# Performance work log

Measured on AMD Instinct MI355X. Metric: run time of the kernel, lower is better.

The kernel has to match this reference:

```python
import jax, jax.numpy as jnp
import numpy as np

B, S, DM, H, DF = 2, 2048, 1024, 16, 4096
HD = DM // H
EPS = 1e-6
NEG = -1e9


def setup_inputs() -> dict:
    key = jax.random.key(0)
    ks = jax.random.split(key, 16)
    sc = 1.0 / np.sqrt(DM)
    scf = 1.0 / np.sqrt(DF)
    return {
        "x": jax.random.normal(ks[0], (B, S, DM), jnp.float32),
        "src_mask": jax.random.randint(ks[1], (B, 1, 1, S), 0, 2, jnp.int32),
        "Wq": jax.random.normal(ks[2], (DM, DM), jnp.float32) * sc,
        "bq": jnp.zeros((DM,), jnp.float32),
        "Wk": jax.random.normal(ks[3], (DM, DM), jnp.float32) * sc,
        "bk": jnp.zeros((DM,), jnp.float32),
        "Wv": jax.random.normal(ks[4], (DM, DM), jnp.float32) * sc,
        "bv": jnp.zeros((DM,), jnp.float32),
        "Wo": jax.random.normal(ks[5], (DM, DM), jnp.float32) * sc,
        "bo": jnp.zeros((DM,), jnp.float32),
        "W1": jax.random.normal(ks[6], (DM, DF), jnp.float32) * sc,
        "b1": jnp.zeros((DF,), jnp.float32),
        "W2": jax.random.normal(ks[7], (DF, DM), jnp.float32) * scf,
        "b2": jnp.zeros((DM,), jnp.float32),
        "alpha1": jnp.ones((1,), jnp.float32),
        "beta1": jnp.ones((1,), jnp.float32),
        "alpha2": jnp.ones((1,), jnp.float32),
        "beta2": jnp.ones((1,), jnp.float32),
    }


def layer_norm(x, alpha, beta):
    # torch: mean + unbiased std (ddof=1), scalar alpha/beta, eps added to std
    mean = jnp.mean(x, axis=-1, keepdims=True)
    std = jnp.std(x, axis=-1, keepdims=True, ddof=1)
    return alpha * (x - mean) / (std + EPS) + beta


def mha(x, mask, Wq, bq, Wk, bk, Wv, bv, Wo, bo):
    def split(t):  # [B,S,DM] -> [B,H,S,HD]
        return t.reshape(B, S, H, HD).transpose(0, 2, 1, 3)
    q = split(x @ Wq + bq)
    k = split(x @ Wk + bk)
    v = split(x @ Wv + bv)
    scores = jnp.einsum("bhqd,bhkd->bhqk", q, k) / np.sqrt(HD)
    scores = jnp.where(mask == 0, NEG, scores)
    probs = jax.nn.softmax(scores, axis=-1)  # dropout in eval mode = identity
    out = jnp.einsum("bhqk,bhkd->bhqd", probs, v)
    out = out.transpose(0, 2, 1, 3).reshape(B, S, DM)
    return out @ Wo + bo


def reference(x, src_mask, Wq, bq, Wk, bk, Wv, bv, Wo, bo, W1, b1, W2, b2,
              alpha1, beta1, alpha2, beta2):
    # pre-norm residual: x + attn(norm(x)); dropout disabled (eval)
    n1 = layer_norm(x, alpha1, beta1)
    h = x + mha(n1, src_mask, Wq, bq, Wk, bk, Wv, bv, Wo, bo)
    n2 = layer_norm(h, alpha2, beta2)
    ff = jax.nn.relu(n2 @ W1 + b1) @ W2 + b2
    return h + ff
```

## Files before the change

### kernel.cpp

```cpp
#include <hip/hip_runtime.h>
#include <hip/hip_bf16.h>

#define SEQ   2048
#define BATCH 2
#define DMODEL 1024
#define DFF   4096
#define NHEAD 16
#define HDIM  64
#define NTOK  (BATCH*SEQ)

typedef short s8v __attribute__((ext_vector_type(8)));
typedef float f4v __attribute__((ext_vector_type(4)));

__device__ __forceinline__ float b2f(unsigned short u) {
    union { unsigned int i; float f; } v; v.i = ((unsigned int)u) << 16; return v.f;
}
__device__ __forceinline__ unsigned short f2b(float f) {
    union { unsigned int i; float f; } v; v.f = f;
    unsigned int r = v.i + 0x7FFFu + ((v.i >> 16) & 1u);
    return (unsigned short)(r >> 16);
}
__device__ __forceinline__ ushort2 cvt_pk(float a, float b) {
    __hip_bfloat162 h = __float22bfloat162_rn(float2{ a, b });
    return *(ushort2*)&h;
}

__device__ __forceinline__ f4v mfma_bf16(s8v a, s8v b, f4v c) {
    return __builtin_amdgcn_mfma_f32_16x16x32_bf16(a, b, c, 0, 0, 0);
}

__device__ __forceinline__ void gload_lds16(const void* g, void* l) {
    __builtin_amdgcn_global_load_lds(
        (const __attribute__((address_space(1))) unsigned int*)g,
        (__attribute__((address_space(3))) unsigned int*)l, 16, 0, 0);
}

template<int N> __device__ __forceinline__ void wait_vmcnt() {
    if constexpr (N == 8)      asm volatile("s_waitcnt vmcnt(8)" ::: "memory");
    else if constexpr (N == 6) asm volatile("s_waitcnt vmcnt(6)" ::: "memory");
    else if constexpr (N == 4) asm volatile("s_waitcnt vmcnt(4)" ::: "memory");
    else if constexpr (N == 2) asm volatile("s_waitcnt vmcnt(2)" ::: "memory");
    else                       asm volatile("s_waitcnt vmcnt(0)" ::: "memory");
}

__device__ __forceinline__ void tp_tile(const float* __restrict__ src,
                                        unsigned short* __restrict__ dst,
                                        int R, int C, int br, int bc, int t,
                                        unsigned short* tl) {
    for (int i = 0; i < 4; i++) {
        int lin = i * 1024 + t * 4;
        int r = lin >> 6, c = lin & 63;
        float4 u = *(const float4*)&src[(size_t)(br * 64 + r) * C + bc * 64 + c];
        tl[r * 65 + c + 0] = f2b(u.x);
        tl[r * 65 + c + 1] = f2b(u.y);
        tl[r * 65 + c + 2] = f2b(u.z);
        tl[r * 65 + c + 3] = f2b(u.w);
    }
    __syncthreads();
    for (int i = 0; i < 4; i++) {
        int lin = i * 1024 + t * 4;
        int r2 = lin >> 6, c2 = lin & 63;
        ushort4 o;
        o.x = tl[(c2 + 0) * 65 + r2];
        o.y = tl[(c2 + 1) * 65 + r2];
        o.z = tl[(c2 + 2) * 65 + r2];
        o.w = tl[(c2 + 3) * 65 + r2];
        *(ushort4*)&dst[(size_t)(bc * 64 + r2) * R + br * 64 + c2] = o;
    }
}

__global__ __launch_bounds__(256) void prep_weights(const float* __restrict__ Wq,
                                                    const float* __restrict__ Wk,
                                                    const float* __restrict__ Wv,
                                                    const float* __restrict__ Wo,
                                                    const float* __restrict__ W1,
                                                    const float* __restrict__ W2,
                                                    const float* __restrict__ bq,
                                                    const float* __restrict__ bk,
                                                    const float* __restrict__ bv,
                                                    const float* __restrict__ x,
                                                    const float* __restrict__ a1,
                                                    const float* __restrict__ be1,
                                                    unsigned short* __restrict__ Wqkv_t,
                                                    unsigned short* __restrict__ Wo_t,
                                                    unsigned short* __restrict__ W1_t,
                                                    unsigned short* __restrict__ W2_t,
                                                    float* __restrict__ bqkv,
                                                    unsigned short* __restrict__ n1) {
    __shared__ unsigned short tl[64 * 65];
    __shared__ float red[8];
    const int t = threadIdx.x;
    const int bx = blockIdx.x, by = blockIdx.y, z = blockIdx.z;
    if (z < 4) {
        const float* src = (z == 0) ? Wq : (z == 1) ? Wk : (z == 2) ? Wv : Wo;
        unsigned short* dst = (z == 3) ? Wo_t : Wqkv_t + (size_t)z * 1024 * 1024;
        tp_tile(src, dst, 1024, 1024, bx, by, t, tl);
    } else if (z == 4) {
        for (int i = 0; i < 4; i++) {
            tp_tile(W1, W1_t, 1024, 4096, bx, by + 16 * i, t, tl);
            __syncthreads();
        }
    } else if (z == 5) {
        if (bx == 0 && by == 0) {
            for (int i = 0; i < 12; i++) {
                int idx = t + 256 * i;
                if (idx < 1024) bqkv[idx] = bq[idx];
                else if (idx < 2048) bqkv[idx] = bk[idx - 1024];
                else if (idx < 3072) bqkv[idx] = bv[idx - 2048];
            }
        }
        for (int i = 0; i < 4; i++) {
            tp_tile(W2, W2_t, 4096, 1024, bx + 16 * i, by, t, tl);
            __syncthreads();
        }
    } else {
        const int row = (z - 6) * 256 + by * 16 + bx;
        const float* xr = x + (size_t)row * DMODEL;
        float4 u = ((const float4*)xr)[t];
        float v[4] = { u.x, u.y, u.z, u.w };
        float s = v[0] + v[1] + v[2] + v[3];
        float sq = v[0]*v[0] + v[1]*v[1] + v[2]*v[2] + v[3]*v[3];
        for (int off = 32; off; off >>= 1) { s += __shfl_xor(s, off); sq += __shfl_xor(sq, off); }
        int wave = t >> 6, lane = t & 63;
        if (!lane) { red[wave] = s; red[4 + wave] = sq; }
        __syncthreads();
        s = red[0] + red[1] + red[2] + red[3];
        sq = red[4] + red[5] + red[6] + red[7];
        float mean = s * (1.f / DMODEL);
        float var = (sq - (float)DMODEL * mean * mean) * (1.f / (DMODEL - 1));
        var = var < 0.f ? 0.f : var;
        float inv = a1[0] / (sqrtf(var) + 1e-6f);
        float bt = be1[0];
        uint2 ou;
        unsigned short r0 = f2b((v[0] - mean) * inv + bt);
        unsigned short r1 = f2b((v[1] - mean) * inv + bt);
        unsigned short r2 = f2b((v[2] - mean) * inv + bt);
        unsigned short r3 = f2b((v[3] - mean) * inv + bt);
        ou.x = (unsigned int)r0 | ((unsigned int)r1 << 16);
        ou.y = (unsigned int)r2 | ((unsigned int)r3 << 16);
        ((uint2*)(n1 + (size_t)row * DMODEL))[t] = ou;
    }
}

__global__ __launch_bounds__(256) void mask_scan(const int* __restrict__ msk,
                                                 int* __restrict__ idx,
                                                 float* __restrict__ maskc2,
                                                 int* __restrict__ ntiles) {
    const int b = blockIdx.x, t = threadIdx.x;
    const int base = b * SEQ;
    __shared__ int wsum[4];
    int k[8]; int cnt = 0;
    for (int j = 0; j < 8; j++) {
        k[j] = (msk[base + t * 8 + j] != 0) ? 1 : 0;
        cnt += k[j];
    }
    const int lane = t & 63, wv = t >> 6;
    int pre = cnt;
    for (int off = 1; off < 64; off <<= 1) {
        int n = __shfl_up(pre, off);
        if (lane >= off) pre += n;
    }
    if (lane == 63) wsum[wv] = pre;
    __syncthreads();
    const int Nb = wsum[0] + wsum[1] + wsum[2] + wsum[3];
    int woff = 0;
    for (int w = 0; w < wv; w++) woff += wsum[w];
    const int excl = woff + pre - cnt;
    for (int j = 0; j < 8; j++) {
        int g = t * 8 + j;
        idx[base + g] = 0;
        maskc2[base + g] = (g < Nb) ? 0.f : -1e9f;
    }
    __syncthreads();
    int pos = excl;
    for (int j = 0; j < 8; j++) {
        if (k[j]) { idx[base + pos] = t * 8 + j; pos++; }
    }
    if (t == 0) ntiles[b] = (Nb + 63) >> 6;
}

__global__ __launch_bounds__(256) void pack_kv(const unsigned short* __restrict__ Kb,
                                               const unsigned short* __restrict__ Vb,
                                               const int* __restrict__ idx,
                                               const int* __restrict__ ntiles,
                                               unsigned short* __restrict__ Kc,
                                               unsigned short* __restrict__ Vc) {
    __shared__ unsigned short tl[64 * 65];
    const int t = threadIdx.x;
    const int kt = blockIdx.x, h = blockIdx.y, b = blockIdx.z;
    if (kt >= ntiles[b]) return;
    const int* idxb = idx + b * SEQ + kt * 64;
    const unsigned short* srcK = Kb + (size_t)b * SEQ * 1024 + h * HDIM;
    unsigned short* dstK = Kc + ((size_t)((b * NHEAD + h) * 32 + kt)) * 4096;
    for (int i = 0; i < 2; i++) {
        int ci = t + 256 * i;
        int r = ci >> 3, cp = ci & 7;
        int cl = cp ^ (r & 7);
        int row = idxb[r];
        *(uint4*)&dstK[ci * 8] = *(const uint4*)&srcK[(size_t)row * 1024 + cl * 8];
    }
    const unsigned short* srcV = Vb + (size_t)b * SEQ * 1024 + h * HDIM;
    for (int i = 0; i < 16; i++) {
        int idx2 = t + 256 * i;
        int r = idx2 >> 6, c = idx2 & 63;
        int row = idxb[r];
        tl[r * 65 + c] = srcV[(size_t)row * 1024 + c];
    }
    __syncthreads();
    unsigned short* dstV = Vc + ((size_t)((b * NHEAD + h) * 32 + kt)) * 4096;
    for (int i = 0; i < 2; i++) {
        int ci = t + 256 * i;
        int r = ci >> 3, cp = ci & 7;
        int cl = cp ^ (r & 7);
        ushort4 e0, e1;
        e0.x = tl[(cl * 8 + 0) * 65 + r]; e0.y = tl[(cl * 8 + 1) * 65 + r];
        e0.z = tl[(cl * 8 + 2) * 65 + r]; e0.w = tl[(cl * 8 + 3) * 65 + r];
        e1.x = tl[(cl * 8 + 4) * 65 + r]; e1.y = tl[(cl * 8 + 5) * 65 + r];
        e1.z = tl[(cl * 8 + 6) * 65 + r]; e1.w = tl[(cl * 8 + 7) * 65 + r];
        *(ushort4*)&dstV[ci * 8]     = e0;
        *(ushort4*)&dstV[ci * 8 + 4] = e1;
    }
}

__global__ __launch_bounds__(256) void ln_add(const float* __restrict__ x,
                                              const float* __restrict__ ws,
                                              const float* __restrict__ al,
                                              const float* __restrict__ be,
                                              float* __restrict__ hb,
                                              unsigned short* __restrict__ o) {
    const int row = blockIdx.x;
    float4 u = ((const float4*)(x + (size_t)row * DMODEL))[threadIdx.x];
    float4 p = ((const float4*)(ws + (size_t)row * DMODEL))[threadIdx.x];
    u.x += p.x; u.y += p.y; u.z += p.z; u.w += p.w;
    ((float4*)(hb + (size_t)row * DMODEL))[threadIdx.x] = u;
    float v[4] = { u.x, u.y, u.z, u.w };
    float s = v[0] + v[1] + v[2] + v[3];
    float sq = v[0]*v[0] + v[1]*v[1] + v[2]*v[2] + v[3]*v[3];
    for (int off = 32; off; off >>= 1) { s += __shfl_xor(s, off); sq += __shfl_xor(sq, off); }
    __shared__ float red[8];
    int wave = threadIdx.x >> 6, lane = threadIdx.x & 63;
    if (!lane) { red[wave] = s; red[4 + wave] = sq; }
    __syncthreads();
    s = red[0] + red[1] + red[2] + red[3];
    sq = red[4] + red[5] + red[6] + red[7];
    float mean = s * (1.f / DMODEL);
    float var = (sq - (float)DMODEL * mean * mean) * (1.f / (DMODEL - 1));
    var = var < 0.f ? 0.f : var;
    float inv = al[0] / (sqrtf(var) + 1e-6f);
    float bt = be[0];
    uint2 ou;
    unsigned short r0 = f2b((v[0] - mean) * inv + bt);
    unsigned short r1 = f2b((v[1] - mean) * inv + bt);
    unsigned short r2 = f2b((v[2] - mean) * inv + bt);
    unsigned short r3 = f2b((v[3] - mean) * inv + bt);
    ou.x = (unsigned int)r0 | ((unsigned int)r1 << 16);
    ou.y = (unsigned int)r2 | ((unsigned int)r3 << 16);
    ((uint2*)(o + (size_t)row * DMODEL))[threadIdx.x] = ou;
}


template<int SPAN, int NL>
__device__ __forceinline__ void stage_half(const unsigned short* __restrict__ mat,
                                           int base, int K, int k0, int q,
                                           unsigned short* sdst, int t) {
#pragma unroll
    for (int i = 0; i < NL; i++) {
        int ci = i * 512 + t;
        int rl = ci >> 3;
        int c  = (ci & 7) ^ (rl & 7);
        int gr = (rl / SPAN) * (2 * SPAN) + q * SPAN + (rl % SPAN);
        gload_lds16(mat + (size_t)(base + gr) * K + k0 + c * 8, sdst + (size_t)ci * 8);
    }
}

__device__ __forceinline__ const s8v* afrag(const unsigned short* sA, int mi, int s,
                                            int wm, int l16, int quad) {
    int q = mi >> 2;
    int rl = wm * 64 + (mi & 3) * 16 + l16;
    return (const s8v*)&sA[q * 8192 + rl * 64 + (((s * 4 + quad) ^ (l16 & 7)) * 8)];
}
__device__ __forceinline__ const s8v* bfrag(const unsigned short* sB, int ni, int s,
                                            int wn, int l16, int quad) {
    int q = ni >> 1;
    int rl = wn * 32 + (ni & 1) * 16 + l16;
    return (const s8v*)&sB[q * 8192 + rl * 64 + (((s * 4 + quad) ^ (l16 & 7)) * 8)];
}

__device__ __forceinline__ void half_8ph(const unsigned short* __restrict__ A,
                                         const unsigned short* __restrict__ Bt,
                                         int m0, int n0, int K, int kT1, int kT2, bool doT2,
                                         const unsigned short* sAr, const unsigned short* sBr,
                                         unsigned short* sA_this, unsigned short* sB_this,
                                         unsigned short* sA_oth,
                                         int wm, int wn, int l16, int quad, int t,
                                         f4v acc[8][4]) {
    s8v a[4][2], b[4][2];
#pragma unroll
    for (int m2 = 0; m2 < 4; m2++) {
        a[m2][0] = *afrag(sAr, m2, 0, wm, l16, quad);
        a[m2][1] = *afrag(sAr, m2, 1, wm, l16, quad);
    }
#pragma unroll
    for (int nb = 0; nb < 2; nb++) {
        b[nb][0] = *bfrag(sBr, nb, 0, wn, l16, quad);
        b[nb][1] = *bfrag(sBr, nb, 1, wn, l16, quad);
    }
    stage_half<64, 2>(A, m0, K, kT1, 1, sA_oth + 8192, t);
    __builtin_amdgcn_s_barrier();
    asm volatile("s_waitcnt lgkmcnt(0)" ::: "memory");
    __builtin_amdgcn_s_setprio(1);
#pragma unroll
    for (int m2 = 0; m2 < 4; m2++)
#pragma unroll
        for (int nb = 0; nb < 2; nb++) {
            acc[m2][nb] = mfma_bf16(a[m2][0], b[nb][0], acc[m2][nb]);
            acc[m2][nb] = mfma_bf16(a[m2][1], b[nb][1], acc[m2][nb]);
        }
    __builtin_amdgcn_s_setprio(0);
    __builtin_amdgcn_s_barrier();
#pragma unroll
    for (int nb = 0; nb < 2; nb++) {
        b[2 + nb][0] = *bfrag(sBr, 2 + nb, 0, wn, l16, quad);
        b[2 + nb][1] = *bfrag(sBr, 2 + nb, 1, wn, l16, quad);
    }
    if (doT2) stage_half<64, 2>(A, m0, K, kT2, 0, sA_this, t);
    __builtin_amdgcn_s_barrier();
    asm volatile("s_waitcnt lgkmcnt(0)" ::: "memory");
    __builtin_amdgcn_s_setprio(1);
#pragma unroll
    for (int m2 = 0; m2 < 4; m2++)
#pragma unroll
        for (int nb = 0; nb < 2; nb++) {
            acc[m2][2 + nb] = mfma_bf16(a[m2][0], b[2 + nb][0], acc[m2][2 + nb]);
            acc[m2][2 + nb] = mfma_bf16(a[m2][1], b[2 + nb][1], acc[m2][2 + nb]);
        }
    __builtin_amdgcn_s_setprio(0);
    __builtin_amdgcn_s_barrier();
#pragma unroll
    for (int m2 = 0; m2 < 4; m2++) {
        a[m2][0] = *afrag(sAr, 4 + m2, 0, wm, l16, quad);
        a[m2][1] = *afrag(sAr, 4 + m2, 1, wm, l16, quad);
    }
    if (doT2) stage_half<32, 2>(Bt, n0, K, kT2, 0, sB_this, t);
    __builtin_amdgcn_s_barrier();
    asm volatile("s_waitcnt lgkmcnt(0)" ::: "memory");
    __builtin_amdgcn_s_setprio(1);
#pragma unroll
    for (int m2 = 0; m2 < 4; m2++)
#pragma unroll
        for (int nb = 0; nb < 2; nb++) {
            acc[4 + m2][nb] = mfma_bf16(a[m2][0], b[nb][0], acc[4 + m2][nb]);
            acc[4 + m2][nb] = mfma_bf16(a[m2][1], b[nb][1], acc[4 + m2][nb]);
        }
    __builtin_amdgcn_s_setprio(0);
    __builtin_amdgcn_s_barrier();
    if (doT2) {
        stage_half<32, 2>(Bt, n0, K, kT2, 1, sB_this + 8192, t);
        wait_vmcnt<6>();
    } else {
        wait_vmcnt<0>();
    }
    __builtin_amdgcn_s_barrier();
    __builtin_amdgcn_s_setprio(1);
#pragma unroll
    for (int m2 = 0; m2 < 4; m2++)
#pragma unroll
        for (int nb = 0; nb < 2; nb++) {
            acc[4 + m2][2 + nb] = mfma_bf16(a[m2][0], b[2 + nb][0], acc[4 + m2][2 + nb]);
            acc[4 + m2][2 + nb] = mfma_bf16(a[m2][1], b[2 + nb][1], acc[4 + m2][2 + nb]);
        }
    __builtin_amdgcn_s_setprio(0);
    __builtin_amdgcn_s_barrier();
}

__device__ __forceinline__ void comp_full(const unsigned short* sA, const unsigned short* sB,
                                          int wm, int wn, int l16, int quad,
                                          f4v acc[8][4]) {
    s8v b[4][2];
#pragma unroll
    for (int ni = 0; ni < 4; ni++) {
        b[ni][0] = *bfrag(sB, ni, 0, wn, l16, quad);
        b[ni][1] = *bfrag(sB, ni, 1, wn, l16, quad);
    }
#pragma unroll
    for (int mi = 0; mi < 8; mi++) {
        s8v a0 = *afrag(sA, mi, 0, wm, l16, quad);
        s8v a1 = *afrag(sA, mi, 1, wm, l16, quad);
#pragma unroll
        for (int ni = 0; ni < 4; ni++) {
            acc[mi][ni] = mfma_bf16(a0, b[ni][0], acc[mi][ni]);
            acc[mi][ni] = mfma_bf16(a1, b[ni][1], acc[mi][ni]);
        }
    }
}

template<bool RELU, typename CT, bool SPLIT3, bool ATOM>
__global__ __launch_bounds__(512, 2) void gemm256(const unsigned short* __restrict__ A,
                                                  const unsigned short* __restrict__ Bt,
                                                  const float* __restrict__ bias,
                                                  CT* __restrict__ C,
                                                  int M, int N, int K, int KS) {
    __shared__ __align__(16) unsigned short smA[2][256 * 64];
    __shared__ __align__(16) unsigned short smB[2][256 * 64];
    const int t = threadIdx.x;
    const int wave = t >> 6, lane = t & 63;
    const int quad = lane >> 4, l16 = lane & 15;
    const int wm = wave >> 2, wn = wave & 3;
    const int m0 = blockIdx.x * 256, n0 = blockIdx.y * 256;
    const int z = blockIdx.z;
    const int kbeg = z * KS;
    const int nt = KS >> 6;

    f4v acc[8][4] = {};

    stage_half<64, 2>(A, m0, K, kbeg, 0, smA[0], t);
    stage_half<64, 2>(A, m0, K, kbeg, 1, smA[0] + 8192, t);
    stage_half<32, 2>(Bt, n0, K, kbeg, 0, smB[0], t);
    stage_half<32, 2>(Bt, n0, K, kbeg, 1, smB[0] + 8192, t);
    stage_half<64, 2>(A, m0, K, kbeg + 64, 0, smA[1], t);
    stage_half<32, 2>(Bt, n0, K, kbeg + 64, 0, smB[1], t);
    stage_half<32, 2>(Bt, n0, K, kbeg + 64, 1, smB[1] + 8192, t);
    wait_vmcnt<6>();
    __builtin_amdgcn_s_barrier();

    for (int i = 0; i < nt / 2 - 1; ++i) {
        const int kb = kbeg + 2 * i * 64;
        half_8ph(A, Bt, m0, n0, K, kb + 64, kb + 128, true,
                 smA[0], smB[0], smA[0], smB[0], smA[1],
                 wm, wn, l16, quad, t, acc);
        half_8ph(A, Bt, m0, n0, K, kb + 128, kb + 192, true,
                 smA[1], smB[1], smA[1], smB[1], smA[0],
                 wm, wn, l16, quad, t, acc);
    }
    half_8ph(A, Bt, m0, n0, K, kbeg + (nt - 1) * 64, 0, false,
             smA[0], smB[0], smA[0], smB[0], smA[1],
             wm, wn, l16, quad, t, acc);
    __builtin_amdgcn_s_setprio(1);
    comp_full(smA[1], smB[1], wm, wn, l16, quad, acc);
    __builtin_amdgcn_s_setprio(0);

#pragma unroll
    for (int mi = 0; mi < 8; mi++) {
#pragma unroll
        for (int ni = 0; ni < 4; ni++) {
            const int col = n0 + wn * 64 + ni * 16 + l16;
            const int row0 = m0 + wm * 128 + mi * 16 + quad * 4;
            const float bv = (!ATOM || z == 0) ? bias[col] : 0.f;
#pragma unroll
            for (int r = 0; r < 4; r++) {
                float v = acc[mi][ni][r] + bv;
                if (RELU) v = v > 0.f ? v : 0.f;
                if constexpr (ATOM) {
                    atomicAdd((float*)&C[(size_t)(row0 + r) * N + col], v);
                } else {
                    size_t cidx;
                    if constexpr (SPLIT3)
                        cidx = (size_t)(col >> 10) * ((size_t)NTOK * 1024)
                             + (size_t)(row0 + r) * 1024 + (col & 1023);
                    else
                        cidx = (size_t)(row0 + r) * N + col;
                    if constexpr (sizeof(CT) == 2)
                        C[cidx] = f2b(v);
                    else
                        C[cidx] = v;
                }
            }
        }
    }
}

#define EXPC 0.18033688f
__device__ __forceinline__ void attn_tile(const unsigned short* __restrict__ smKb,
                                          const unsigned short* __restrict__ smVb,
                                          const float* __restrict__ smM, int k0,
                                          unsigned short* __restrict__ smPw,
                                          s8v qf0, s8v qf1, int quad, int l16,
                                          float& l_s, f4v* oacc) {
    const int l7 = l16 & 7;
    f4v s[4];
#pragma unroll
    for (int kt4 = 0; kt4 < 4; kt4++) {
        int r = kt4 * 16 + l16;
        s8v kf0 = *(const s8v*)&smKb[r * 64 + ((quad ^ l7) * 8)];
        s8v kf1 = *(const s8v*)&smKb[r * 64 + (((quad + 4) ^ l7) * 8)];
        f4v z = {};
        z = mfma_bf16(kf0, qf0, z);
        z = mfma_bf16(kf1, qf1, z);
        s[kt4] = z;
    }
#pragma unroll
    for (int kt4 = 0; kt4 < 4; kt4++) {
        float4 mf = *(const float4*)&smM[k0 + kt4 * 16 + quad * 4];
        s[kt4][0] = s[kt4][0] * EXPC + mf.x;
        s[kt4][1] = s[kt4][1] * EXPC + mf.y;
        s[kt4][2] = s[kt4][2] * EXPC + mf.z;
        s[kt4][3] = s[kt4][3] * EXPC + mf.w;
    }
#pragma unroll
    for (int kt4 = 0; kt4 < 4; kt4++)
#pragma unroll
        for (int r = 0; r < 4; r++) {
            float p = __builtin_amdgcn_exp2f(s[kt4][r]);
            s[kt4][r] = p;
            l_s += p;
        }
#pragma unroll
    for (int kt4 = 0; kt4 < 4; kt4++) {
        ushort2 p01 = cvt_pk(s[kt4][0], s[kt4][1]);
        ushort2 p23 = cvt_pk(s[kt4][2], s[kt4][3]);
        ushort4 pk;
        pk.x = p01.x; pk.y = p01.y; pk.z = p23.x; pk.w = p23.y;
        int c = kt4 * 2 + (quad >> 1);
        *(ushort4*)&smPw[l16 * 64 + ((c ^ l7) * 8 + (quad & 1) * 4)] = pk;
    }
    s8v pf0 = *(const s8v*)&smPw[l16 * 64 + ((quad ^ l7) * 8)];
    s8v pf1 = *(const s8v*)&smPw[l16 * 64 + (((quad + 4) ^ l7) * 8)];
#pragma unroll
    for (int nt = 0; nt < 4; nt++) {
        int r = nt * 16 + l16;
        s8v v0 = *(const s8v*)&smVb[r * 64 + ((quad ^ l7) * 8)];
        s8v v1 = *(const s8v*)&smVb[r * 64 + (((quad + 4) ^ l7) * 8)];
        oacc[nt] = mfma_bf16(pf0, v0, oacc[nt]);
        oacc[nt] = mfma_bf16(pf1, v1, oacc[nt]);
    }
}

__global__ __launch_bounds__(512) void attn_kernel(const unsigned short* __restrict__ Qb,
                                                   const unsigned short* __restrict__ Kc,
                                                   const unsigned short* __restrict__ Vc,
                                                   const float* __restrict__ maskc2,
                                                   const int* __restrict__ ntiles,
                                                   unsigned short* __restrict__ out) {
    __shared__ __align__(16) unsigned short smK[2][4096];
    __shared__ __align__(16) unsigned short smV[2][4096];
    __shared__ __align__(16) unsigned short smP[8][1024];
    __shared__ __align__(16) float smM[SEQ];

    const int t = threadIdx.x;
    const int wave = t >> 6, lane = t & 63;
    const int quad = lane >> 4, l16 = lane & 15;
    const int qt = blockIdx.x, h = blockIdx.y, b = blockIdx.z;
    const int q0 = qt * 128 + wave * 16;
    const int nt = ntiles[b];
    const unsigned short* Kbh = Kc + ((size_t)(b * NHEAD + h)) * 32 * 4096;
    const unsigned short* Vbh = Vc + ((size_t)(b * NHEAD + h)) * 32 * 4096;
    unsigned short* smPw = &smP[wave][0];

    const unsigned short* Qp = Qb + ((size_t)b * SEQ + q0 + l16) * 1024 + h * HDIM + quad * 8;
    s8v qf0 = *(const s8v*)(Qp);
    s8v qf1 = *(const s8v*)(Qp + 32);

    gload_lds16(maskc2 + (size_t)b * SEQ + t * 4, (float*)smM + t * 4);
    gload_lds16(Kbh + t * 8,        smK[0] + t * 8);
    gload_lds16(Vbh + t * 8,        smV[0] + t * 8);
    gload_lds16(Kbh + 4096 + t * 8, smK[1] + t * 8);
    gload_lds16(Vbh + 4096 + t * 8, smV[1] + t * 8);
    wait_vmcnt<2>();
    __builtin_amdgcn_s_barrier();

    float l_s = 0.f;
    f4v oacc[4] = {};

    for (int it = 0; it < nt; ++it) {
        const int cb = it & 1;
        __builtin_amdgcn_s_setprio(1);
        attn_tile(smK[cb], smV[cb], smM, it * 64, smPw, qf0, qf1, quad, l16, l_s, oacc);
        __builtin_amdgcn_s_setprio(0);
        if (it + 2 < nt) {
            asm volatile("s_waitcnt lgkmcnt(0)" ::: "memory");
            __builtin_amdgcn_s_barrier();
            gload_lds16(Kbh + (size_t)(it + 2) * 4096 + t * 8, smK[cb] + t * 8);
            gload_lds16(Vbh + (size_t)(it + 2) * 4096 + t * 8, smV[cb] + t * 8);
            wait_vmcnt<2>();
            __builtin_amdgcn_s_barrier();
        } else if (it + 1 < nt) {
            asm volatile("s_waitcnt lgkmcnt(0)" ::: "memory");
            __builtin_amdgcn_s_barrier();
            wait_vmcnt<0>();
            __builtin_amdgcn_s_barrier();
        }
    }

    l_s += __shfl_xor(l_s, 16);
    l_s += __shfl_xor(l_s, 32);
    float lrr[4];
    for (int r = 0; r < 4; r++) lrr[r] = __shfl(l_s, quad * 4 + r);
    for (int nt2 = 0; nt2 < 4; nt2++)
        for (int r = 0; r < 4; r++) {
            int row = q0 + quad * 4 + r;
            int col = h * HDIM + nt2 * 16 + l16;
            out[((size_t)b * SEQ + row) * DMODEL + col] = f2b(oacc[nt2][r] / lrr[r]);
        }
}

extern "C" void kernel_launch(void* const* d_in, const int* in_sizes, int n_in,
                              void* d_out, int out_size, void* d_ws, size_t ws_size,
                              hipStream_t stream) {
    const float* x   = (const float*)d_in[0];
    const int*   msk = (const int*)d_in[1];
    const float* Wq  = (const float*)d_in[2];
    const float* bq  = (const float*)d_in[3];
    const float* Wk  = (const float*)d_in[4];
    const float* bk  = (const float*)d_in[5];
    const float* Wv  = (const float*)d_in[6];
    const float* bv  = (const float*)d_in[7];
    const float* Wo  = (const float*)d_in[8];
    const float* bo  = (const float*)d_in[9];
    const float* W1  = (const float*)d_in[10];
    const float* b1  = (const float*)d_in[11];
    const float* W2  = (const float*)d_in[12];
    const float* b2  = (const float*)d_in[13];
    const float* a1  = (const float*)d_in[14];
    const float* be1 = (const float*)d_in[15];
    const float* a2  = (const float*)d_in[16];
    const float* be2 = (const float*)d_in[17];
    float* outf = (float*)d_out;

    char* ws = (char*)d_ws;
    const size_t MB = 1024 * 1024;
    unsigned short* W2_t   = (unsigned short*)(ws);
    unsigned short* W1_t   = (unsigned short*)(ws + 8 * MB);
    unsigned short* Wqkv_t = (unsigned short*)(ws + 16 * MB);
    float*          bqkv   = (float*)(ws + 22 * MB);
    unsigned short* Kc     = (unsigned short*)(ws + 16 * MB);
    unsigned short* n2     = (unsigned short*)(ws + 16 * MB);
    unsigned short* Wo_t   = (unsigned short*)(ws + 24 * MB);
    unsigned short* Qb     = (unsigned short*)(ws + 26 * MB);
    unsigned short* Kb     = (unsigned short*)(ws + 34 * MB);
    unsigned short* Vb     = (unsigned short*)(ws + 42 * MB);
    float*          wsum   = (float*)(ws + 34 * MB);
    unsigned short* ff1    = (unsigned short*)(ws + 26 * MB);
    unsigned short* attnO  = (unsigned short*)(ws + 50 * MB);
    unsigned short* n1     = (unsigned short*)d_out;
    unsigned short* Vc     = (unsigned short*)d_out;
    float*          hbuf   = (float*)d_out;
    float*          maskc2 = (float*)((char*)d_out + 8 * MB);
    int*            idxc   = (int*)((char*)d_out + 8 * MB + 16 * 1024);
    int*            ntl    = (int*)((char*)d_out + 8 * MB + 32 * 1024);

    mask_scan<<<dim3(BATCH), 256, 0, stream>>>(msk, idxc, maskc2, ntl);
    prep_weights<<<dim3(16, 16, 22), 256, 0, stream>>>(
        Wq, Wk, Wv, Wo, W1, W2, bq, bk, bv, x, a1, be1,
        Wqkv_t, Wo_t, W1_t, W2_t, bqkv, n1);

    gemm256<false, unsigned short, true, false><<<dim3(16, 12, 1), 512, 0, stream>>>(
        n1, Wqkv_t, bqkv, Qb, NTOK, 3072, 1024, 1024);
    pack_kv<<<dim3(32, 16, 2), 256, 0, stream>>>(Kb, Vb, idxc, ntl, Kc, Vc);
    hipMemsetAsync(wsum, 0, (size_t)NTOK * DMODEL * sizeof(float), stream);
    attn_kernel<<<dim3(16, 16, 2), 512, 0, stream>>>(Qb, Kc, Vc, maskc2, ntl, attnO);
    gemm256<false, float, false, true><<<dim3(16, 4, 4), 512, 0, stream>>>(
        attnO, Wo_t, bo, wsum, NTOK, 1024, 1024, 256);
    ln_add<<<NTOK, 256, 0, stream>>>(x, wsum, a2, be2, hbuf, n2);
    gemm256<true, unsigned short, false, false><<<dim3(16, 16, 1), 512, 0, stream>>>(
        n2, W1_t, b1, ff1, NTOK, DFF, 1024, 1024);
    gemm256<false, float, false, true><<<dim3(16, 4, 4), 512, 0, stream>>>(
        ff1, W2_t, b2, outf, NTOK, 1024, 4096, 1024);
}
```

Before: 391.3 us.

## Replace atomic split-K GEMMs with 128-tile two-way split and fused residual

The Wo and W2 projections move from 256x256 tiles with 4-way atomicAdd split-K onto a new 128x128 kernel. That kernel splits K two ways across blocks and also across wave groups inside a block, then reduces the wave groups through shared memory. Block z=0 writes bias plus residual straight into the output, and z=1 writes a partial buffer that ln_add or a new add_pbuf kernel folds in afterwards. This removes the memset and the float atomics, and fuses the residual add. In exchange it adds an extra elementwise pass, partial-buffer traffic, and a smaller tile with less reuse per block.

After: 327.5 us. 1.19x faster.

```diff
diff --git a/kernel.cpp b/kernel.cpp
--- a/kernel.cpp
+++ b/kernel.cpp
@@ -222,17 +222,18 @@
     }
 }
 
-__global__ __launch_bounds__(256) void ln_add(const float* __restrict__ x,
-                                              const float* __restrict__ ws,
+__global__ __launch_bounds__(256) void ln_add(float* __restrict__ hb,
+                                              const float* __restrict__ pbuf,
                                               const float* __restrict__ al,
                                               const float* __restrict__ be,
-                                              float* __restrict__ hb,
                                               unsigned short* __restrict__ o) {
     const int row = blockIdx.x;
-    float4 u = ((const float4*)(x + (size_t)row * DMODEL))[threadIdx.x];
-    float4 p = ((const float4*)(ws + (size_t)row * DMODEL))[threadIdx.x];
+    float* hr = hb + (size_t)row * DMODEL;
+    const float* pr = pbuf + (size_t)row * DMODEL;
+    float4 u = ((const float4*)hr)[threadIdx.x];
+    float4 p = ((const float4*)pr)[threadIdx.x];
     u.x += p.x; u.y += p.y; u.z += p.z; u.w += p.w;
-    ((float4*)(hb + (size_t)row * DMODEL))[threadIdx.x] = u;
+    ((float4*)hr)[threadIdx.x] = u;
     float v[4] = { u.x, u.y, u.z, u.w };
     float s = v[0] + v[1] + v[2] + v[3];
     float sq = v[0]*v[0] + v[1]*v[1] + v[2]*v[2] + v[3]*v[3];
@@ -258,6 +259,18 @@
     ((uint2*)(o + (size_t)row * DMODEL))[threadIdx.x] = ou;
 }
 
+__global__ __launch_bounds__(256) void add_pbuf(float* __restrict__ out,
+                                                const float* __restrict__ pbuf) {
+    const int i0 = (blockIdx.x * 256 + threadIdx.x) * 8;
+    float4 a0 = *(const float4*)&out[i0];
+    float4 a1 = *(const float4*)&out[i0 + 4];
+    float4 p0 = *(const float4*)&pbuf[i0];
+    float4 p1 = *(const float4*)&pbuf[i0 + 4];
+    a0.x += p0.x; a0.y += p0.y; a0.z += p0.z; a0.w += p0.w;
+    a1.x += p1.x; a1.y += p1.y; a1.z += p1.z; a1.w += p1.w;
+    *(float4*)&out[i0]     = a0;
+    *(float4*)&out[i0 + 4] = a1;
+}
 
 template<int SPAN, int NL>
 __device__ __forceinline__ void stage_half(const unsigned short* __restrict__ mat,
@@ -394,12 +407,12 @@
     }
 }
 
-template<bool RELU, typename CT, bool SPLIT3, bool ATOM>
+template<bool RELU, typename CT, bool SPLIT3>
 __global__ __launch_bounds__(512, 2) void gemm256(const unsigned short* __restrict__ A,
                                                   const unsigned short* __restrict__ Bt,
                                                   const float* __restrict__ bias,
                                                   CT* __restrict__ C,
-                                                  int M, int N, int K, int KS) {
+                                                  int M, int N, int K) {
     __shared__ __align__(16) unsigned short smA[2][256 * 64];
     __shared__ __align__(16) unsigned short smB[2][256 * 64];
     const int t = threadIdx.x;
@@ -407,24 +420,22 @@
     const int quad = lane >> 4, l16 = lane & 15;
     const int wm = wave >> 2, wn = wave & 3;
     const int m0 = blockIdx.x * 256, n0 = blockIdx.y * 256;
-    const int z = blockIdx.z;
-    const int kbeg = z * KS;
-    const int nt = KS >> 6;
+    const int nt = K >> 6;
 
     f4v acc[8][4] = {};
 
-    stage_half<64, 2>(A, m0, K, kbeg, 0, smA[0], t);
-    stage_half<64, 2>(A, m0, K, kbeg, 1, smA[0] + 8192, t);
-    stage_half<32, 2>(Bt, n0, K, kbeg, 0, smB[0], t);
-    stage_half<32, 2>(Bt, n0, K, kbeg, 1, smB[0] + 8192, t);
-    stage_half<64, 2>(A, m0, K, kbeg + 64, 0, smA[1], t);
-    stage_half<32, 2>(Bt, n0, K, kbeg + 64, 0, smB[1], t);
-    stage_half<32, 2>(Bt, n0, K, kbeg + 64, 1, smB[1] + 8192, t);
+    stage_half<64, 2>(A, m0, K, 0, 0, smA[0], t);
+    stage_half<64, 2>(A, m0, K, 0, 1, smA[0] + 8192, t);
+    stage_half<32, 2>(Bt, n0, K, 0, 0, smB[0], t);
+    stage_half<32, 2>(Bt, n0, K, 0, 1, smB[0] + 8192, t);
+    stage_half<64, 2>(A, m0, K, 64, 0, smA[1], t);
+    stage_half<32, 2>(Bt, n0, K, 64, 0, smB[1], t);
+    stage_half<32, 2>(Bt, n0, K, 64, 1, smB[1] + 8192, t);
     wait_vmcnt<6>();
     __builtin_amdgcn_s_barrier();
 
     for (int i = 0; i < nt / 2 - 1; ++i) {
-        const int kb = kbeg + 2 * i * 64;
+        const int kb = 2 * i * 64;
         half_8ph(A, Bt, m0, n0, K, kb + 64, kb + 128, true,
                  smA[0], smB[0], smA[0], smB[0], smA[1],
                  wm, wn, l16, quad, t, acc);
@@ -432,7 +443,7 @@
                  smA[1], smB[1], smA[1], smB[1], smA[0],
                  wm, wn, l16, quad, t, acc);
     }
-    half_8ph(A, Bt, m0, n0, K, kbeg + (nt - 1) * 64, 0, false,
+    half_8ph(A, Bt, m0, n0, K, (nt - 1) * 64, 0, false,
              smA[0], smB[0], smA[0], smB[0], smA[1],
              wm, wn, l16, quad, t, acc);
     __builtin_amdgcn_s_setprio(1);
@@ -445,27 +456,135 @@
         for (int ni = 0; ni < 4; ni++) {
             const int col = n0 + wn * 64 + ni * 16 + l16;
             const int row0 = m0 + wm * 128 + mi * 16 + quad * 4;
-            const float bv = (!ATOM || z == 0) ? bias[col] : 0.f;
+            const float bv = bias[col];
 #pragma unroll
             for (int r = 0; r < 4; r++) {
                 float v = acc[mi][ni][r] + bv;
                 if (RELU) v = v > 0.f ? v : 0.f;
-                if constexpr (ATOM) {
-                    atomicAdd((float*)&C[(size_t)(row0 + r) * N + col], v);
+                size_t cidx;
+                if constexpr (SPLIT3)
+                    cidx = (size_t)(col >> 10) * ((size_t)NTOK * 1024)
+                         + (size_t)row0 * 1024 + (size_t)r * 1024 + (col & 1023);
+                else
+                    cidx = (size_t)(row0 + r) * N + col;
+                if constexpr (sizeof(CT) == 2)
+                    C[cidx] = f2b(v);
+                else
+                    C[cidx] = v;
+            }
+        }
+    }
+}
+
+
+__device__ __forceinline__ void stage128(const unsigned short* __restrict__ mat,
+                                         int base, int K, int k0,
+                                         unsigned short* sdst, int t) {
+#pragma unroll
+    for (int q = 0; q < 2; q++) {
+        int rl = t >> 3;
+        int c  = (t & 7) ^ (rl & 7);
+        gload_lds16(mat + (size_t)(base + q * 64 + rl) * K + k0 + c * 8,
+                    sdst + q * 4096 + (size_t)t * 8);
+    }
+}
+
+__device__ __forceinline__ s8v rdfrag128(const unsigned short* sm, int q, int fi,
+                                         int l16, int quad, int sW) {
+    int rl = fi * 16 + l16;
+    int p = (sW * 4 + quad) ^ (l16 & 7);
+    return *(const s8v*)&sm[q * 4096 + rl * 64 + p * 8];
+}
+
+__global__ __launch_bounds__(512, 4) void gemm128k(const unsigned short* __restrict__ A,
+                                                   const unsigned short* __restrict__ Bt,
+                                                   const float* __restrict__ bias,
+                                                   const float* __restrict__ res,
+                                                   float* __restrict__ C,
+                                                   float* __restrict__ pbuf,
+                                                   int M, int N, int K, int KS) {
+    __shared__ __align__(16) unsigned short smem[4][8192];
+    const int t = threadIdx.x;
+    const int wave = t >> 6, lane = t & 63;
+    const int quad = lane >> 4, l16 = lane & 15;
+    const int sW = wave >> 2, wm = (wave >> 1) & 1, wn = wave & 1;
+    const int m0 = blockIdx.x * 128, n0 = blockIdx.y * 128;
+    const int z = blockIdx.z;
+    const int kbeg = z * KS;
+    const int nt = KS >> 6;
+
+    f4v acc[4][4] = {};
+
+    stage128(A,  m0, K, kbeg,      smem[0], t);
+    stage128(Bt, n0, K, kbeg,      smem[2], t);
+    stage128(A,  m0, K, kbeg + 64, smem[1], t);
+    stage128(Bt, n0, K, kbeg + 64, smem[3], t);
+    wait_vmcnt<4>();
+    __builtin_amdgcn_s_barrier();
+
+    for (int it = 0; it < nt; ++it) {
+        const int cb = it & 1;
+        const unsigned short* sA = smem[cb];
+        const unsigned short* sB = smem[2 + cb];
+        s8v a[4], b[4];
+#pragma unroll
+        for (int i = 0; i < 4; i++) a[i] = rdfrag128(sA, wm, i, l16, quad, sW);
+#pragma unroll
+        for (int i = 0; i < 4; i++) b[i] = rdfrag128(sB, wn, i, l16, quad, sW);
+        asm volatile("s_waitcnt lgkmcnt(0)" ::: "memory");
+        __builtin_amdgcn_s_setprio(1);
+#pragma unroll
+        for (int mi = 0; mi < 4; mi++)
+#pragma unroll
+            for (int ni = 0; ni < 4; ni++)
+                acc[mi][ni] = mfma_bf16(a[mi], b[ni], acc[mi][ni]);
+        __builtin_amdgcn_s_setprio(0);
+        __builtin_amdgcn_s_barrier();
+        if (it + 2 < nt) {
+            stage128(A,  m0, K, kbeg + (it + 2) * 64, smem[cb], t);
+            stage128(Bt, n0, K, kbeg + (it + 2) * 64, smem[2 + cb], t);
+            wait_vmcnt<4>();
+        } else if (it + 1 < nt) {
+            wait_vmcnt<0>();
+        }
+        __builtin_amdgcn_s_barrier();
+    }
+
+    float* xch = (float*)&smem[0][0];
+    float* myx = xch + (wm * 2 + wn) * 4096;
+    if (sW == 1) {
+#pragma unroll
+        for (int mi = 0; mi < 4; mi++)
+#pragma unroll
+            for (int ni = 0; ni < 4; ni++)
+                *(f4v*)&myx[(mi * 4 + ni) * 256 + lane * 4] = acc[mi][ni];
+    }
+    __builtin_amdgcn_s_barrier();
+    if (sW == 0) {
+#pragma unroll
+        for (int mi = 0; mi < 4; mi++)
+#pragma unroll
+            for (int ni = 0; ni < 4; ni++)
+                acc[mi][ni] += *(const f4v*)&myx[(mi * 4 + ni) * 256 + lane * 4];
+#pragma unroll
+        for (int mi = 0; mi < 4; mi++)
+#pragma unroll
+            for (int ni = 0; ni < 4; ni++) {
+                const int col = n0 + wn * 64 + ni * 16 + l16;
+                const int row0 = m0 + wm * 64 + mi * 16 + quad * 4;
+                if (z == 0) {
+                    const float bv = bias[col];
+#pragma unroll
+                    for (int r = 0; r < 4; r++) {
+                        size_t ix = (size_t)(row0 + r) * N + col;
+                        C[ix] = acc[mi][ni][r] + bv + res[ix];
+                    }
                 } else {
-                    size_t cidx;
-                    if constexpr (SPLIT3)
-                        cidx = (size_t)(col >> 10) * ((size_t)NTOK * 1024)
-                             + (size_t)(row0 + r) * 1024 + (col & 1023);
-                    else
-                        cidx = (size_t)(row0 + r) * N + col;
-                    if constexpr (sizeof(CT) == 2)
-                        C[cidx] = f2b(v);
-                    else
-                        C[cidx] = v;
+#pragma unroll
+                    for (int r = 0; r < 4; r++)
+                        pbuf[(size_t)(row0 + r) * N + col] = acc[mi][ni][r];
                 }
             }
-        }
     }
 }
 
@@ -620,6 +739,7 @@
     const size_t MB = 1024 * 1024;
     unsigned short* W2_t   = (unsigned short*)(ws);
     unsigned short* W1_t   = (unsigned short*)(ws + 8 * MB);
+    float*          Pbuf   = (float*)(ws + 8 * MB);
     unsigned short* Wqkv_t = (unsigned short*)(ws + 16 * MB);
     float*          bqkv   = (float*)(ws + 22 * MB);
     unsigned short* Kc     = (unsigned short*)(ws + 16 * MB);
@@ -628,7 +748,7 @@
     unsigned short* Qb     = (unsigned short*)(ws + 26 * MB);
     unsigned short* Kb     = (unsigned short*)(ws + 34 * MB);
     unsigned short* Vb     = (unsigned short*)(ws + 42 * MB);
-    float*          wsum   = (float*)(ws + 34 * MB);
+    float*          Pbuf2  = (float*)(ws + 34 * MB);
     unsigned short* ff1    = (unsigned short*)(ws + 26 * MB);
     unsigned short* attnO  = (unsigned short*)(ws + 50 * MB);
     unsigned short* n1     = (unsigned short*)d_out;
@@ -643,16 +763,16 @@
         Wq, Wk, Wv, Wo, W1, W2, bq, bk, bv, x, a1, be1,
         Wqkv_t, Wo_t, W1_t, W2_t, bqkv, n1);
 
-    gemm256<false, unsigned short, true, false><<<dim3(16, 12, 1), 512, 0, stream>>>(
-        n1, Wqkv_t, bqkv, Qb, NTOK, 3072, 1024, 1024);
+    gemm256<false, unsigned short, true><<<dim3(16, 12), 512, 0, stream>>>(
+        n1, Wqkv_t, bqkv, Qb, NTOK, 3072, 1024);
     pack_kv<<<dim3(32, 16, 2), 256, 0, stream>>>(Kb, Vb, idxc, ntl, Kc, Vc);
-    hipMemsetAsync(wsum, 0, (size_t)NTOK * DMODEL * sizeof(float), stream);
     attn_kernel<<<dim3(16, 16, 2), 512, 0, stream>>>(Qb, Kc, Vc, maskc2, ntl, attnO);
-    gemm256<false, float, false, true><<<dim3(16, 4, 4), 512, 0, stream>>>(
-        attnO, Wo_t, bo, wsum, NTOK, 1024, 1024, 256);
-    ln_add<<<NTOK, 256, 0, stream>>>(x, wsum, a2, be2, hbuf, n2);
-    gemm256<true, unsigned short, false, false><<<dim3(16, 16, 1), 512, 0, stream>>>(
-        n2, W1_t, b1, ff1, NTOK, DFF, 1024, 1024);
-    gemm256<false, float, false, true><<<dim3(16, 4, 4), 512, 0, stream>>>(
-        ff1, W2_t, b2, outf, NTOK, 1024, 4096, 1024);
-}
+    gemm128k<<<dim3(32, 8, 2), 512, 0, stream>>>(
+        attnO, Wo_t, bo, x, hbuf, Pbuf2, NTOK, 1024, 1024, 512);
+    ln_add<<<NTOK, 256, 0, stream>>>(hbuf, Pbuf2, a2, be2, n2);
+    gemm256<true, unsigned short, false><<<dim3(16, 16), 512, 0, stream>>>(
+        n2, W1_t, b1, ff1, NTOK, DFF, 1024);
+    gemm128k<<<dim3(32, 8, 2), 512, 0, stream>>>(
+        ff1, W2_t, b2, hbuf, outf, Pbuf, NTOK, 1024, 4096, 2048);
+    add_pbuf<<<dim3(2048), 256, 0, stream>>>(outf, Pbuf);
+}
```
